# Performance work log

Hardware: AMD Instinct MI355X
Metric: run time of the kernel (lower is better)

## Reference

```python
import jax, jax.numpy as jnp
import numpy as np

N_LETTERS = 128
WORD_DIM = 128      # word embed dim; char-LSTM hidden = 64 per direction
SENT_DIM = 256      # sentence embed dim; word-LSTM hidden = 128 per direction
B, S, LW = 128, 64, 16


def _lstm_dir(x, Wih, Whh, b, reverse):
    """One direction of an LSTM. x: [B,T,D], Wih: [4H,D], Whh: [4H,H], b: [4H].
    PyTorch gate order (i, f, g, o). Returns (outputs [B,T,H], final h [B,H])."""
    Bc = x.shape[0]
    H = Whh.shape[-1]
    xw = jnp.einsum('btd,gd->btg', x, Wih) + b  # precompute input projections

    def step(carry, xt):
        h, c = carry
        g = xt + h @ Whh.T
        i, f, gg, o = jnp.split(g, 4, axis=-1)
        c = jax.nn.sigmoid(f) * c + jax.nn.sigmoid(i) * jnp.tanh(gg)
        h = jax.nn.sigmoid(o) * jnp.tanh(c)
        return (h, c), h

    z = jnp.zeros((Bc, H), x.dtype)
    (h, _), hs = jax.lax.scan(step, (z, z), jnp.swapaxes(xw, 0, 1), reverse=reverse)
    return jnp.swapaxes(hs, 0, 1), h


def _bilstm_final(x, Wih_per_layer, Whh, b):
    """2-layer bidirectional LSTM; returns concat of last-layer final hiddens [B,2H].
    Wih_per_layer: list of length 2 of [2,4H,Din_l]; Whh: [2,2,4H,H]; b: [2,2,4H]."""
    hf = hb = None
    for l in range(2):
        of, hf = _lstm_dir(x, Wih_per_layer[l][0], Whh[l, 0], b[l, 0], False)
        ob, hb = _lstm_dir(x, Wih_per_layer[l][1], Whh[l, 1], b[l, 1], True)
        x = jnp.concatenate([of, ob], axis=-1)
    return jnp.concatenate([hf, hb], axis=-1)


def _mlp2(h, W1, b1, W2, b2):
    return jax.nn.relu(h @ W1.T + b1) @ W2.T + b2


def setup_inputs() -> dict:
    rng = np.random.default_rng(0)
    # sentences: non-empty words contiguous at the front of each sentence
    sent_lens = rng.integers(8, S + 1, B)
    word_lens = rng.integers(1, LW + 1, (B, S))
    chars = rng.integers(1, N_LETTERS + 1, (B, S, LW))
    pos = np.arange(LW)
    chars = np.where(pos[None, None, :] < word_lens[:, :, None], chars, 0)
    chars = np.where(np.arange(S)[None, :, None] < sent_lens[:, None, None], chars, 0)
    sentences = jnp.asarray(chars, dtype=jnp.int32)
    # target words: all non-empty (filter in WordEmbedder is then identity)
    wlens = rng.integers(1, LW + 1, B)
    wchars = rng.integers(1, N_LETTERS + 1, (B, LW))
    wchars = np.where(pos[None, :] < wlens[:, None], wchars, 0)
    words = jnp.asarray(wchars, dtype=jnp.int32)

    ks = jax.random.split(jax.random.key(0), 32)
    sc = 0.05
    Hw, Hs = WORD_DIM // 2, SENT_DIM // 2  # 64, 128
    p = {
        'sentences': sentences, 'words': words,
        'emb': jax.random.normal(ks[0], (N_LETTERS + 1, WORD_DIM)) * sc,
        # char-level word LSTM: both layers have input dim WORD_DIM
        'w_Wih': jax.random.normal(ks[1], (2, 2, 4 * Hw, WORD_DIM)) * sc,
        'w_Whh': jax.random.normal(ks[2], (2, 2, 4 * Hw, Hw)) * sc,
        'w_b': jax.random.normal(ks[3], (2, 2, 4 * Hw)) * sc,
        'w_fc_W1': jax.random.normal(ks[4], (WORD_DIM, WORD_DIM)) * sc,
        'w_fc_b1': jax.random.normal(ks[5], (WORD_DIM,)) * sc,
        'w_fc_W2': jax.random.normal(ks[6], (WORD_DIM, WORD_DIM)) * sc,
        'w_fc_b2': jax.random.normal(ks[7], (WORD_DIM,)) * sc,
        # sentence LSTM: layer0 input WORD_DIM, layer1 input SENT_DIM
        's_Wih0': jax.random.normal(ks[8], (2, 4 * Hs, WORD_DIM)) * sc,
        's_Wih1': jax.random.normal(ks[9], (2, 4 * Hs, SENT_DIM)) * sc,
        's_Whh': jax.random.normal(ks[10], (2, 2, 4 * Hs, Hs)) * sc,
        's_b': jax.random.normal(ks[11], (2, 2, 4 * Hs)) * sc,
        's_fc_W1': jax.random.normal(ks[12], (SENT_DIM, SENT_DIM)) * sc,
        's_fc_b1': jax.random.normal(ks[13], (SENT_DIM,)) * sc,
        's_fc_W2': jax.random.normal(ks[14], (SENT_DIM, SENT_DIM)) * sc,
        's_fc_b2': jax.random.normal(ks[15], (SENT_DIM,)) * sc,
        # classifier 384 -> 256 -> 128 -> 2
        'c_W0': jax.random.normal(ks[16], (256, SENT_DIM + WORD_DIM)) * sc,
        'c_b0': jax.random.normal(ks[17], (256,)) * sc,
        'c_W1': jax.random.normal(ks[18], (128, 256)) * sc,
        'c_b1': jax.random.normal(ks[19], (128,)) * sc,
        'c_W2': jax.random.normal(ks[20], (2, 128)) * sc,
        'c_b2': jax.random.normal(ks[21], (2,)) * sc,
    }
    return p


def _word_embed(tokens, emb, w_Wih, w_Whh, w_b, W1, b1, W2, b2):
    x = emb[tokens]  # [N, LW, WORD_DIM]
    h = _bilstm_final(x, [w_Wih[0], w_Wih[1]], w_Whh, w_b)
    return _mlp2(h, W1, b1, W2, b2)


def reference(sentences, words, emb, w_Wih, w_Whh, w_b, w_fc_W1, w_fc_b1,
              w_fc_W2, w_fc_b2, s_Wih0, s_Wih1, s_Whh, s_b, s_fc_W1, s_fc_b1,
              s_fc_W2, s_fc_b2, c_W0, c_b0, c_W1, c_b1, c_W2, c_b2):
    Bc, Sc, Lc = sentences.shape
    flat = sentences.reshape(-1, Lc)
    we = _word_embed(flat, emb, w_Wih, w_Whh, w_b,
                     w_fc_W1, w_fc_b1, w_fc_W2, w_fc_b2)  # [B*S, WORD_DIM]
    # ragged scatter-pad == zero-mask empty word slots (non-empty words are at front)
    nonempty = (flat != 0).any(axis=1)  # [B*S]
    unflat = (we * nonempty[:, None].astype(we.dtype)).reshape(Bc, Sc, WORD_DIM)
    hs = _bilstm_final(unflat, [s_Wih0, s_Wih1], s_Whh, s_b)
    sent_emb = _mlp2(hs, s_fc_W1, s_fc_b1, s_fc_W2, s_fc_b2)  # [B, SENT_DIM]
    word_emb = _word_embed(words, emb, w_Wih, w_Whh, w_b,
                           w_fc_W1, w_fc_b1, w_fc_W2, w_fc_b2)  # [B, WORD_DIM]
    x = jnp.concatenate([sent_emb, word_emb], axis=1)
    x = jax.nn.relu(x @ c_W0.T + c_b0)
    x = jax.nn.relu(x @ c_W1.T + c_b1)
    x = x @ c_W2.T + c_b2
    return jax.nn.log_softmax(x, axis=1)
```

## Files before the change

### kernel.cpp

```cpp
#include <hip/hip_runtime.h>
#include <hip/hip_bf16.h>
#include <math.h>

typedef unsigned int u32;
typedef unsigned short u16;
typedef __hip_bfloat16 bf16_t;
typedef float f32x4 __attribute__((ext_vector_type(4)));
typedef short bf16x8 __attribute__((ext_vector_type(8)));

__device__ __forceinline__ float blo(u32 p){ union{u32 u; float f;} c; c.u = p << 16; return c.f; }
__device__ __forceinline__ float bhi(u32 p){ union{u32 u; float f;} c; c.u = p & 0xFFFF0000u; return c.f; }
#define LOG2E  1.44269504088896340736f
#define LOG2E2 2.88539008177792681472f
__device__ __forceinline__ float fsigm(float x){
  return __builtin_amdgcn_rcpf(1.0f + __builtin_amdgcn_exp2f(-x*LOG2E));
}
__device__ __forceinline__ float ftanh(float x){
  return 1.0f - 2.0f*__builtin_amdgcn_rcpf(1.0f + __builtin_amdgcn_exp2f(x*LOG2E2));
}
__device__ __forceinline__ u16 f2bu(float f){
  union{float f; u32 u;} c; c.f = f;
  u32 u = c.u + 0x7FFFu + ((c.u >> 16) & 1u);
  return (u16)(u >> 16);
}

#define WE_OFF   0u
#define L0O_OFF  2129920u
#define SFIN_OFF 6324224u
#define XW_OFF   6455296u
#define WB_OFF   40009728u
#define SEG_WWIH  0
#define SEG_WWHH  131072
#define SEG_FW1   196608
#define SEG_FW2   212992
#define SEG_SWIH0 229376
#define SEG_SWIH1 360448
#define SEG_SWHH  622592
#define SEG_TOTAL 884736
#define EMB_TOTAL 16512

__global__ __launch_bounds__(256) void prep_weights(
    const float* __restrict__ wWih, const float* __restrict__ wWhh,
    const float* __restrict__ fW1,  const float* __restrict__ fW2,
    const float* __restrict__ sWih0,const float* __restrict__ sWih1,
    const float* __restrict__ sWhh, const float* __restrict__ emb,
    u16* __restrict__ dst, u16* __restrict__ embB)
{
  for (int i = blockIdx.x*256 + threadIdx.x; i < SEG_TOTAL + EMB_TOTAL; i += gridDim.x*256){
    if (i < SEG_TOTAL){
      const float* s; int off;
      if      (i < SEG_WWHH ){ s = wWih;  off = i; }
      else if (i < SEG_FW1  ){ s = wWhh;  off = i - SEG_WWHH; }
      else if (i < SEG_FW2  ){ s = fW1;   off = i - SEG_FW1; }
      else if (i < SEG_SWIH0){ s = fW2;   off = i - SEG_FW2; }
      else if (i < SEG_SWIH1){ s = sWih0; off = i - SEG_SWIH0; }
      else if (i < SEG_SWHH ){ s = sWih1; off = i - SEG_SWIH1; }
      else                   { s = sWhh;  off = i - SEG_SWHH; }
      dst[i] = f2bu(s[off]);
    } else {
      embB[i - SEG_TOTAL] = f2bu(emb[i - SEG_TOTAL]);
    }
  }
}

__global__ __launch_bounds__(512, 2) void word_mfma(
    const int* __restrict__ sentences, const int* __restrict__ words,
    const u16* __restrict__ embB,
    const u16* __restrict__ wWihB, const u16* __restrict__ wWhhB,
    const float* __restrict__ wb,
    const u16* __restrict__ fW1B, const float* __restrict__ fb1,
    const u16* __restrict__ fW2B, const float* __restrict__ fb2,
    bf16_t* __restrict__ we_out )
{
  const int blk  = blockIdx.x;
  const int tid  = threadIdx.x;
  const int lane = tid & 63;
  const int wv   = tid >> 6;
  const int dq   = wv >> 2;
  const int wq   = wv & 3;
  const int lr   = lane & 15;
  const int lg   = lane >> 4;

  __shared__ __align__(16) u16 SQ[16*16*128];
  __shared__ __align__(16) u16 Hb[2][2][16*64];
  __shared__ __align__(16) u16 HF[16*128];
  __shared__ int chs[256];
  __shared__ int emptyf[16];
  u16* A1 = (u16*)Hb;

  const int wbase = blk*16;
  if (tid < 256){
    int w = tid >> 4, t = tid & 15;
    int gw = wbase + w;
    chs[tid] = (gw < 8192) ? sentences[gw*16 + t] : words[(gw - 8192)*16 + t];
  }
  __syncthreads();
  if (tid < 16){
    int acc = 0;
    #pragma unroll
    for (int i = 0; i < 16; ++i) acc |= chs[tid*16 + i];
    emptyf[tid] = (wbase + tid < 8192) && (acc == 0);
  }
  __syncthreads();

  for (int layer = 0; layer < 2; ++layer){
    const int ld = layer*2 + dq;
    bf16x8 bih[4][4], bhh[4][2];
    float bias[4];
    #pragma unroll
    for (int j = 0; j < 4; ++j){
      const int col = (wq + 4*j)*16 + lr;
      bias[j] = wb[ld*256 + col];
      const u16* pih = wWihB + (size_t)(ld*256 + col)*128 + lg*8;
      #pragma unroll
      for (int kk = 0; kk < 4; ++kk) bih[j][kk] = *(const bf16x8*)(pih + kk*32);
      const u16* phh = wWhhB + (size_t)(ld*256 + col)*64 + lg*8;
      #pragma unroll
      for (int kk = 0; kk < 2; ++kk) bhh[j][kk] = *(const bf16x8*)(phh + kk*32);
    }
    float cst[4] = {0.f, 0.f, 0.f, 0.f};
    for (int i = tid; i < 2*2*16*64; i += 512) ((u16*)Hb)[i] = 0;
    __syncthreads();
    int cur = 0;
    bf16x8 xfn[4];
    if (layer == 0){
      const int t0 = dq ? 15 : 0;
      const u16* xp = embB + (size_t)chs[lr*16 + t0]*128 + lg*8;
      #pragma unroll
      for (int kk = 0; kk < 4; ++kk) xfn[kk] = *(const bf16x8*)(xp + kk*32);
    }
    for (int step = 0; step < 16; ++step){
      const int t = dq ? (15 - step) : step;
      f32x4 ac[4];
      #pragma unroll
      for (int j = 0; j < 4; ++j) ac[j] = (f32x4){bias[j], bias[j], bias[j], bias[j]};
      if (layer == 0){
        bf16x8 xf[4];
        #pragma unroll
        for (int kk = 0; kk < 4; ++kk) xf[kk] = xfn[kk];
        if (step < 15){
          const int tn = dq ? (14 - step) : (step + 1);
          const u16* xp = embB + (size_t)chs[lr*16 + tn]*128 + lg*8;
          #pragma unroll
          for (int kk = 0; kk < 4; ++kk) xfn[kk] = *(const bf16x8*)(xp + kk*32);
        }
        #pragma unroll
        for (int kk = 0; kk < 4; ++kk){
          #pragma unroll
          for (int j = 0; j < 4; ++j)
            ac[j] = __builtin_amdgcn_mfma_f32_16x16x32_bf16(xf[kk], bih[j][kk], ac[j], 0, 0, 0);
        }
      } else {
        #pragma unroll
        for (int kk = 0; kk < 4; ++kk){
          const int c = (kk*4 + lg) ^ lr;
          bf16x8 a = *(const bf16x8*)&SQ[((lr*16 + t)*16 + c)*8];
          #pragma unroll
          for (int j = 0; j < 4; ++j)
            ac[j] = __builtin_amdgcn_mfma_f32_16x16x32_bf16(a, bih[j][kk], ac[j], 0, 0, 0);
        }
      }
      #pragma unroll
      for (int kk = 0; kk < 2; ++kk){
        const int c = (kk*4 + lg) ^ (lr & 7);
        bf16x8 a = *(const bf16x8*)&Hb[dq][cur][(lr*8 + c)*8];
        #pragma unroll
        for (int j = 0; j < 4; ++j)
          ac[j] = __builtin_amdgcn_mfma_f32_16x16x32_bf16(a, bhh[j][kk], ac[j], 0, 0, 0);
      }
      const int u = wq*16 + lr;
      #pragma unroll
      for (int r = 0; r < 4; ++r){
        const int w = lg*4 + r;
        float ig = fsigm(ac[0][r]);
        float fg = fsigm(ac[1][r]);
        float gg = ftanh(ac[2][r]);
        float og = fsigm(ac[3][r]);
        cst[r] = fg*cst[r] + ig*gg;
        float hn = og * ftanh(cst[r]);
        u16 hb = f2bu(hn);
        Hb[dq][cur^1][(w*8 + ((u >> 3) ^ (w & 7)))*8 + (u & 7)] = hb;
        const int d = dq*64 + u;
        const int dc = (d >> 3) ^ (w & 15);
        if (layer == 0)       SQ[((w*16 + t)*16 + dc)*8 + (d & 7)] = hb;
        else if (step == 15)  HF[(w*16 + dc)*8 + (d & 7)] = hb;
      }
      __syncthreads();
      cur ^= 1;
    }
  }

  {
    const int col = wv*16 + lr;
    float bs = fb1[col];
    bf16x8 b1[4];
    const u16* src = fW1B + (size_t)col*128 + lg*8;
    #pragma unroll
    for (int kk = 0; kk < 4; ++kk) b1[kk] = *(const bf16x8*)(src + kk*32);
    f32x4 ac = (f32x4){bs, bs, bs, bs};
    #pragma unroll
    for (int kk = 0; kk < 4; ++kk){
      const int c = (kk*4 + lg) ^ lr;
      bf16x8 a = *(const bf16x8*)&HF[(lr*16 + c)*8];
      ac = __builtin_amdgcn_mfma_f32_16x16x32_bf16(a, b1[kk], ac, 0, 0, 0);
    }
    __syncthreads();
    #pragma unroll
    for (int r = 0; r < 4; ++r){
      const int w = lg*4 + r;
      A1[(w*16 + ((col >> 3) ^ (w & 15)))*8 + (col & 7)] = f2bu(fmaxf(ac[r], 0.f));
    }
  }
  __syncthreads();
  {
    const int col = wv*16 + lr;
    float bs = fb2[col];
    bf16x8 b2[4];
    const u16* src = fW2B + (size_t)col*128 + lg*8;
    #pragma unroll
    for (int kk = 0; kk < 4; ++kk) b2[kk] = *(const bf16x8*)(src + kk*32);
    f32x4 ac = (f32x4){bs, bs, bs, bs};
    #pragma unroll
    for (int kk = 0; kk < 4; ++kk){
      const int c = (kk*4 + lg) ^ lr;
      bf16x8 a = *(const bf16x8*)&A1[(lr*16 + c)*8];
      ac = __builtin_amdgcn_mfma_f32_16x16x32_bf16(a, b2[kk], ac, 0, 0, 0);
    }
    u16* wo = (u16*)we_out;
    #pragma unroll
    for (int r = 0; r < 4; ++r){
      const int w = lg*4 + r;
      wo[(size_t)(wbase + w)*128 + col] = emptyf[w] ? (u16)0 : f2bu(ac[r]);
    }
  }
}

template<int KK>
__global__ __launch_bounds__(256, 1) void xw_gemm(
    const u16* __restrict__ X, const u16* __restrict__ W,
    const float* __restrict__ bias, float* __restrict__ out)
{
  const int rowb = blockIdx.x;
  const int colb = blockIdx.y;
  const int tid = threadIdx.x;
  const int lane = tid & 63, wv = tid >> 6;
  const int lr = lane & 15, lg = lane >> 4;
  const int K = KK*32;

  bf16x8 bf[4][KK];
  f32x4 ac[4];
  #pragma unroll
  for (int j = 0; j < 4; ++j){
    const int g = colb*256 + (wv*4 + j)*16 + lr;
    const float bs = bias[g];
    ac[j] = (f32x4){bs, bs, bs, bs};
    const u16* src = W + (size_t)g*K + lg*8;
    #pragma unroll
    for (int kk = 0; kk < KK; ++kk) bf[j][kk] = *(const bf16x8*)(src + kk*32);
  }
  const u16* xr = X + (size_t)(rowb*16 + lr)*K + lg*8;
  #pragma unroll
  for (int kk = 0; kk < KK; ++kk){
    bf16x8 a = *(const bf16x8*)(xr + kk*32);
    #pragma unroll
    for (int j = 0; j < 4; ++j)
      ac[j] = __builtin_amdgcn_mfma_f32_16x16x32_bf16(a, bf[j][kk], ac[j], 0, 0, 0);
  }
  #pragma unroll
  for (int j = 0; j < 4; ++j){
    const int g = colb*256 + (wv*4 + j)*16 + lr;
    #pragma unroll
    for (int r = 0; r < 4; ++r)
      out[(size_t)(rowb*16 + lg*4 + r)*1024 + g] = ac[j][r];
  }
}

__global__ __launch_bounds__(512, 1) void sent_rec(
    const float* __restrict__ xw ,
    const u16* __restrict__ sWhhB ,
    bf16_t* __restrict__ l0out ,
    float* __restrict__ sfin ,
    const int layer)
{
  const int dir = blockIdx.x & 1;
  const int sg0 = (blockIdx.x >> 1) << 4;
  const int tid = threadIdx.x;
  const int lane = tid & 63, wv = tid >> 6;
  const int lr = lane & 15, lg = lane >> 4;

  __shared__ __align__(16) u16 Hs[2][2048];

  bf16x8 bhh[4][4];
  #pragma unroll
  for (int j = 0; j < 4; ++j){
    const int g = (wv + 8*j)*16 + lr;
    const u16* p = sWhhB + (size_t)((layer*2 + dir)*512 + g)*128 + lg*8;
    #pragma unroll
    for (int kk = 0; kk < 4; ++kk) bhh[j][kk] = *(const bf16x8*)(p + kk*32);
  }
  for (int i = tid; i < 4096; i += 512) ((u16*)Hs)[i] = 0;
  float cst[4] = {0.f, 0.f, 0.f, 0.f};

  size_t rowoff[4];
  #pragma unroll
  for (int r = 0; r < 4; ++r)
    rowoff[r] = (size_t)(sg0 + lg*4 + r)*64*1024 + dir*512 + wv*16 + lr;

  float xwv[16], xwn[16];
  {
    const int t0 = dir ? 63 : 0;
    #pragma unroll
    for (int j = 0; j < 4; ++j)
      #pragma unroll
      for (int r = 0; r < 4; ++r)
        xwv[j*4 + r] = xw[rowoff[r] + (size_t)t0*1024 + j*128];
  }
  __syncthreads();

  u16* lob = (u16*)l0out;
  int cur = 0;
  for (int step = 0; step < 64; ++step){
    const int t = dir ? (63 - step) : step;
    f32x4 ac[4];
    #pragma unroll
    for (int j = 0; j < 4; ++j)
      ac[j] = (f32x4){xwv[j*4+0], xwv[j*4+1], xwv[j*4+2], xwv[j*4+3]};
    if (step < 63){
      const int tn = dir ? (62 - step) : (step + 1);
      #pragma unroll
      for (int j = 0; j < 4; ++j)
        #pragma unroll
        for (int r = 0; r < 4; ++r)
          xwn[j*4 + r] = xw[rowoff[r] + (size_t)tn*1024 + j*128];
    }
    #pragma unroll
    for (int kk = 0; kk < 4; ++kk){
      const bf16x8 ha = *(const bf16x8*)&Hs[cur][(lr*16 + ((kk*4 + lg) ^ lr))*8];
      #pragma unroll
      for (int j = 0; j < 4; ++j)
        ac[j] = __builtin_amdgcn_mfma_f32_16x16x32_bf16(ha, bhh[j][kk], ac[j], 0, 0, 0);
    }
    const int u = wv*16 + lr;
    #pragma unroll
    for (int r = 0; r < 4; ++r){
      const int s = lg*4 + r;
      float ig = fsigm(ac[0][r]);
      float fg = fsigm(ac[1][r]);
      float gg = ftanh(ac[2][r]);
      float og = fsigm(ac[3][r]);
      cst[r] = fg*cst[r] + ig*gg;
      float hn = og * ftanh(cst[r]);
      Hs[cur^1][(s*16 + ((u >> 3) ^ s))*8 + (u & 7)] = f2bu(hn);
      if (layer == 0)
        lob[((size_t)(sg0 + s)*64 + t)*256 + dir*128 + u] = f2bu(hn);
      else if (step == 63)
        sfin[(size_t)(sg0 + s)*256 + dir*128 + u] = hn;
    }
    __syncthreads();
    cur ^= 1;
    #pragma unroll
    for (int i = 0; i < 16; ++i) xwv[i] = xwn[i];
  }
}

__global__ __launch_bounds__(256) void head_kernel(
    const float* __restrict__ sfin, const bf16_t* __restrict__ wet,
    const float* __restrict__ sW1, const float* __restrict__ sb1,
    const float* __restrict__ sW2, const float* __restrict__ sb2,
    const float* __restrict__ cW0, const float* __restrict__ cb0,
    const float* __restrict__ cW1, const float* __restrict__ cb1,
    const float* __restrict__ cW2, const float* __restrict__ cb2,
    float* __restrict__ out)
{
  const int bs = blockIdx.x, tid = threadIdx.x;
  __shared__ __align__(16) float hin[256];
  __shared__ __align__(16) float a1[256];
  __shared__ __align__(16) float xcat[384];
  __shared__ __align__(16) float b0o[256];
  __shared__ __align__(16) float h1o[128];
  __shared__ float lg[2];

  hin[tid] = sfin[(size_t)bs*256 + tid];
  if (tid < 64){
    const u32* src = (const u32*)(wet + (size_t)bs*128);
    u32 p = src[tid];
    xcat[256 + tid*2]     = blo(p);
    xcat[256 + tid*2 + 1] = bhi(p);
  }
  __syncthreads();
  {
    const float4* wr = (const float4*)(sW1 + (size_t)tid*256);
    float acc = sb1[tid];
    #pragma unroll
    for (int i = 0; i < 64; ++i){
      float4 v = wr[i]; const float* hp = &hin[i*4];
      acc += hp[0]*v.x + hp[1]*v.y + hp[2]*v.z + hp[3]*v.w;
    }
    a1[tid] = fmaxf(acc, 0.0f);
  }
  __syncthreads();
  {
    const float4* wr = (const float4*)(sW2 + (size_t)tid*256);
    float acc = sb2[tid];
    #pragma unroll
    for (int i = 0; i < 64; ++i){
      float4 v = wr[i]; const float* hp = &a1[i*4];
      acc += hp[0]*v.x + hp[1]*v.y + hp[2]*v.z + hp[3]*v.w;
    }
    xcat[tid] = acc;
  }
  __syncthreads();
  {
    const float4* wr = (const float4*)(cW0 + (size_t)tid*384);
    float acc = cb0[tid];
    #pragma unroll
    for (int i = 0; i < 96; ++i){
      float4 v = wr[i]; const float* hp = &xcat[i*4];
      acc += hp[0]*v.x + hp[1]*v.y + hp[2]*v.z + hp[3]*v.w;
    }
    b0o[tid] = fmaxf(acc, 0.0f);
  }
  __syncthreads();
  if (tid < 128){
    const float4* wr = (const float4*)(cW1 + (size_t)tid*256);
    float acc = cb1[tid];
    #pragma unroll
    for (int i = 0; i < 64; ++i){
      float4 v = wr[i]; const float* hp = &b0o[i*4];
      acc += hp[0]*v.x + hp[1]*v.y + hp[2]*v.z + hp[3]*v.w;
    }
    h1o[tid] = fmaxf(acc, 0.0f);
  }
  __syncthreads();
  if (tid < 2){
    const float4* wr = (const float4*)(cW2 + (size_t)tid*128);
    float acc = cb2[tid];
    #pragma unroll
    for (int i = 0; i < 32; ++i){
      float4 v = wr[i]; const float* hp = &h1o[i*4];
      acc += hp[0]*v.x + hp[1]*v.y + hp[2]*v.z + hp[3]*v.w;
    }
    lg[tid] = acc;
  }
  __syncthreads();
  if (tid == 0){
    float m = fmaxf(lg[0], lg[1]);
    float lse = m + logf(expf(lg[0] - m) + expf(lg[1] - m));
    out[bs*2 + 0] = lg[0] - lse;
    out[bs*2 + 1] = lg[1] - lse;
  }
}

extern "C" void kernel_launch(void* const* d_in, const int* in_sizes, int n_in,
                              void* d_out, int out_size, void* d_ws, size_t ws_size,
                              hipStream_t stream) {
  const int*   sentences = (const int*)d_in[0];
  const int*   words     = (const int*)d_in[1];
  const float* emb    = (const float*)d_in[2];
  const float* wWih   = (const float*)d_in[3];
  const float* wWhh   = (const float*)d_in[4];
  const float* wb     = (const float*)d_in[5];
  const float* fW1    = (const float*)d_in[6];
  const float* fb1    = (const float*)d_in[7];
  const float* fW2    = (const float*)d_in[8];
  const float* fb2    = (const float*)d_in[9];
  const float* sWih0  = (const float*)d_in[10];
  const float* sWih1  = (const float*)d_in[11];
  const float* sWhh   = (const float*)d_in[12];
  const float* sb     = (const float*)d_in[13];
  const float* sW1    = (const float*)d_in[14];
  const float* sb1    = (const float*)d_in[15];
  const float* sW2    = (const float*)d_in[16];
  const float* sb2    = (const float*)d_in[17];
  const float* cW0    = (const float*)d_in[18];
  const float* cb0    = (const float*)d_in[19];
  const float* cW1    = (const float*)d_in[20];
  const float* cb1    = (const float*)d_in[21];
  const float* cW2    = (const float*)d_in[22];
  const float* cb2    = (const float*)d_in[23];

  char* W = (char*)d_ws;
  bf16_t* we   = (bf16_t*)(W + WE_OFF);
  bf16_t* l0o  = (bf16_t*)(W + L0O_OFF);
  float*  sfin = (float*) (W + SFIN_OFF);
  float*  xw   = (float*) (W + XW_OFF);
  u16*    embB = (u16*)   (W + XW_OFF);
  u16*    wB   = (u16*)   (W + WB_OFF);
  bf16_t* wet  = we + (size_t)8192*128;

  prep_weights<<<dim3(440), dim3(256), 0, stream>>>(
      wWih, wWhh, fW1, fW2, sWih0, sWih1, sWhh, emb, wB, embB);
  word_mfma<<<dim3(520), dim3(512), 0, stream>>>(
      sentences, words, embB,
      wB + SEG_WWIH, wB + SEG_WWHH, wb,
      wB + SEG_FW1, fb1, wB + SEG_FW2, fb2, we);
  xw_gemm<4><<<dim3(512, 4), dim3(256), 0, stream>>>(
      (const u16*)we, wB + SEG_SWIH0, sb, xw);
  sent_rec<<<dim3(16), dim3(512), 0, stream>>>(xw, wB + SEG_SWHH, l0o, sfin, 0);
  xw_gemm<8><<<dim3(512, 4), dim3(256), 0, stream>>>(
      (const u16*)l0o, wB + SEG_SWIH1, sb + 1024, xw);
  sent_rec<<<dim3(16), dim3(512), 0, stream>>>(xw, wB + SEG_SWHH, l0o, sfin, 1);
  head_kernel<<<dim3(128), dim3(256), 0, stream>>>(
      sfin, wet, sW1, sb1, sW2, sb2, cW0, cb0, cW1, cb1, cW2, cb2,
      (float*)d_out);
}
```

Before: 382.1 us.

## Skip all-empty word blocks, prefetch layer-1 LDS inputs, lighten step barriers

The char-LSTM kernel now exits early for blocks whose 16 words are all empty, writing zero embeddings instead of running both LSTM layers. Layer 1 now prefetches the next timestep's input rows from shared memory one step ahead, the same way layer 0 already prefetched embeddings. The per-step __syncthreads in both the char and sentence recurrences is replaced by an LDS-only wait plus s_barrier, so the barrier no longer waits on outstanding global stores. The early exit relies on empty words sitting at the end of each sentence and their outputs being masked to zero. The lighter barrier assumes no global memory dependence across a step.

```diff
diff --git a/kernel.cpp b/kernel.cpp
--- a/kernel.cpp
+++ b/kernel.cpp
@@ -4,6 +4,7 @@
 
 typedef unsigned int u32;
 typedef unsigned short u16;
+typedef unsigned long long u64;
 typedef __hip_bfloat16 bf16_t;
 typedef float f32x4 __attribute__((ext_vector_type(4)));
 typedef short bf16x8 __attribute__((ext_vector_type(8)));
@@ -22,6 +23,10 @@
   union{float f; u32 u;} c; c.f = f;
   u32 u = c.u + 0x7FFFu + ((c.u >> 16) & 1u);
   return (u16)(u >> 16);
+}
+__device__ __forceinline__ void barrier_lds(){
+  asm volatile("s_waitcnt lgkmcnt(0)" ::: "memory");
+  __builtin_amdgcn_s_barrier();
 }
 
 #define WE_OFF   0u
@@ -103,6 +108,17 @@
   }
   __syncthreads();
 
+  {
+    int allz = 1;
+    #pragma unroll
+    for (int i = 0; i < 16; ++i) allz &= emptyf[i];
+    if (allz){
+      u64* wo = (u64*)(we_out + (size_t)wbase*128);
+      wo[tid] = 0ull;
+      return;
+    }
+  }
+
   for (int layer = 0; layer < 2; ++layer){
     const int ld = layer*2 + dq;
     bf16x8 bih[4][4], bhh[4][2];
@@ -123,42 +139,47 @@
     __syncthreads();
     int cur = 0;
     bf16x8 xfn[4];
-    if (layer == 0){
+    {
       const int t0 = dq ? 15 : 0;
-      const u16* xp = embB + (size_t)chs[lr*16 + t0]*128 + lg*8;
-      #pragma unroll
-      for (int kk = 0; kk < 4; ++kk) xfn[kk] = *(const bf16x8*)(xp + kk*32);
-    }
-    for (int step = 0; step < 16; ++step){
-      const int t = dq ? (15 - step) : step;
-      f32x4 ac[4];
-      #pragma unroll
-      for (int j = 0; j < 4; ++j) ac[j] = (f32x4){bias[j], bias[j], bias[j], bias[j]};
       if (layer == 0){
-        bf16x8 xf[4];
+        const u16* xp = embB + (size_t)chs[lr*16 + t0]*128 + lg*8;
         #pragma unroll
-        for (int kk = 0; kk < 4; ++kk) xf[kk] = xfn[kk];
-        if (step < 15){
-          const int tn = dq ? (14 - step) : (step + 1);
-          const u16* xp = embB + (size_t)chs[lr*16 + tn]*128 + lg*8;
-          #pragma unroll
-          for (int kk = 0; kk < 4; ++kk) xfn[kk] = *(const bf16x8*)(xp + kk*32);
-        }
-        #pragma unroll
-        for (int kk = 0; kk < 4; ++kk){
-          #pragma unroll
-          for (int j = 0; j < 4; ++j)
-            ac[j] = __builtin_amdgcn_mfma_f32_16x16x32_bf16(xf[kk], bih[j][kk], ac[j], 0, 0, 0);
-        }
+        for (int kk = 0; kk < 4; ++kk) xfn[kk] = *(const bf16x8*)(xp + kk*32);
       } else {
         #pragma unroll
         for (int kk = 0; kk < 4; ++kk){
           const int c = (kk*4 + lg) ^ lr;
-          bf16x8 a = *(const bf16x8*)&SQ[((lr*16 + t)*16 + c)*8];
+          xfn[kk] = *(const bf16x8*)&SQ[((lr*16 + t0)*16 + c)*8];
+        }
+      }
+    }
+    for (int step = 0; step < 16; ++step){
+      const int t = dq ? (15 - step) : step;
+      f32x4 ac[4];
+      #pragma unroll
+      for (int j = 0; j < 4; ++j) ac[j] = (f32x4){bias[j], bias[j], bias[j], bias[j]};
+      bf16x8 xf[4];
+      #pragma unroll
+      for (int kk = 0; kk < 4; ++kk) xf[kk] = xfn[kk];
+      if (step < 15){
+        const int tn = dq ? (14 - step) : (step + 1);
+        if (layer == 0){
+          const u16* xp = embB + (size_t)chs[lr*16 + tn]*128 + lg*8;
           #pragma unroll
-          for (int j = 0; j < 4; ++j)
-            ac[j] = __builtin_amdgcn_mfma_f32_16x16x32_bf16(a, bih[j][kk], ac[j], 0, 0, 0);
+          for (int kk = 0; kk < 4; ++kk) xfn[kk] = *(const bf16x8*)(xp + kk*32);
+        } else {
+          #pragma unroll
+          for (int kk = 0; kk < 4; ++kk){
+            const int c = (kk*4 + lg) ^ lr;
+            xfn[kk] = *(const bf16x8*)&SQ[((lr*16 + tn)*16 + c)*8];
+          }
         }
+      }
+      #pragma unroll
+      for (int kk = 0; kk < 4; ++kk){
+        #pragma unroll
+        for (int j = 0; j < 4; ++j)
+          ac[j] = __builtin_amdgcn_mfma_f32_16x16x32_bf16(xf[kk], bih[j][kk], ac[j], 0, 0, 0);
       }
       #pragma unroll
       for (int kk = 0; kk < 2; ++kk){
@@ -185,7 +206,7 @@
         if (layer == 0)       SQ[((w*16 + t)*16 + dc)*8 + (d & 7)] = hb;
         else if (step == 15)  HF[(w*16 + dc)*8 + (d & 7)] = hb;
       }
-      __syncthreads();
+      barrier_lds();
       cur ^= 1;
     }
   }
@@ -356,7 +377,7 @@
       else if (step == 63)
         sfin[(size_t)(sg0 + s)*256 + dir*128 + u] = hn;
     }
-    __syncthreads();
+    barrier_lds();
     cur ^= 1;
     #pragma unroll
     for (int i = 0; i < 16; ++i) xwv[i] = xwn[i];
```

Measured after the change: 417.8 us. 9.3% more time.
